# Performance work log

Hardware: AMD Instinct MI355X
Metric: run time of the kernel (lower is better)

The kernel has to match this reference:

```python
import jax, jax.numpy as jnp
import numpy as np

D_MODEL = 1024
D_INNER = 2048   # expand * d_model
D_STATE = 16
DT_RANK = 64     # ceil(d_model / 16)
D_CONV = 4
L = 2048
EPS = 1e-5


def setup_inputs() -> dict:
    key = jax.random.key(0)
    ks = jax.random.split(key, 8)
    sc = lambda k, shape: jax.random.normal(k, shape, jnp.float32) * 0.02
    A = jnp.tile(jnp.arange(1, D_STATE + 1, dtype=jnp.float32), (D_INNER, 1))
    return {
        "x": jax.random.normal(ks[0], (L, D_MODEL), jnp.float32),
        "W_in": sc(ks[1], (D_MODEL, 2 * D_INNER)),          # in_proj (no bias)
        "W_conv": sc(ks[2], (D_CONV, D_INNER)),             # depthwise conv kernel
        "b_conv": jnp.zeros((D_INNER,), jnp.float32),
        "W_x": sc(ks[3], (D_INNER, DT_RANK + 2 * D_STATE)), # x_proj (no bias)
        "W_dt": sc(ks[4], (DT_RANK, D_INNER)),
        "b_dt": jnp.zeros((D_INNER,), jnp.float32),
        "A_log": jnp.log(A),
        "D": jnp.ones((D_INNER,), jnp.float32),
        "W_out": sc(ks[5], (D_INNER, D_MODEL)),             # out_proj (no bias)
        "ln_scale": jnp.ones((D_MODEL,), jnp.float32),
        "ln_bias": jnp.zeros((D_MODEL,), jnp.float32),
        "drop_key": 0,  # unused: training=False -> DropPath is identity
    }


def reference(x, W_in, W_conv, b_conv, W_x, W_dt, b_dt, A_log, D, W_out,
              ln_scale, ln_bias, drop_key):
    l = x.shape[0]
    # LayerNorm (flax default: mean/var over features)
    mu = jnp.mean(x, axis=-1, keepdims=True)
    var = jnp.mean(jnp.square(x), axis=-1, keepdims=True) - jnp.square(mu)
    xn = (x - mu) * jax.lax.rsqrt(var + EPS) * ln_scale + ln_bias

    # MambaBlock
    xr = xn @ W_in                         # (l, 2*d_inner)
    u, res = xr[:, :D_INNER], xr[:, D_INNER:]

    # causal depthwise conv: pad left d_conv-1, take first l outputs
    up = jnp.pad(u, ((D_CONV - 1, 0), (0, 0)))
    uc = b_conv + sum(up[k:k + l] * W_conv[k] for k in range(D_CONV))
    u2 = jax.nn.silu(uc)                   # (l, d_inner)

    # SSM params (input-dependent)
    x_dbl = u2 @ W_x                       # (l, dt_rank + 2n)
    dt = x_dbl[:, :DT_RANK]
    B = x_dbl[:, DT_RANK:DT_RANK + D_STATE]
    C = x_dbl[:, DT_RANK + D_STATE:]
    delta = jax.nn.softplus(dt @ W_dt + b_dt)   # (l, d_inner)
    A = -jnp.exp(A_log)                         # (d_inner, n)

    dA = jnp.exp(jnp.einsum('ld,dn->ldn', delta, A))   # (l, d_inner, n)
    dBu = jnp.einsum('ld,ln->ldn', delta * u2, B)       # (l, d_inner, n)

    def step(h, inp):
        dA_t, dBu_t, C_t = inp
        h = dA_t * h + dBu_t               # (d_inner, n)
        return h, h @ C_t                  # y_t: (d_inner,)

    h0 = jnp.zeros((D_INNER, D_STATE), dtype=u2.dtype)
    _, ys = jax.lax.scan(step, h0, (dA, dBu, C))
    y = ys + u2 * D                        # (l, d_inner)

    y = y * jax.nn.silu(res)
    out = y @ W_out                        # (l, d_model)
    return out + x                         # residual (DropPath identity in eval)
```

## Files before the change

kernel.cpp:

```cpp
#include <hip/hip_runtime.h>
#include <math.h>

#define L_SEQ 2048
#define DM 1024
#define DI 2048
#define DS 16
#define DTR 64
#define EPS 1e-5f
#define NSEG 32
#define SEGLEN 64
#define NSTATE (DI * DS)

typedef float f32x4 __attribute__((ext_vector_type(4)));
typedef __bf16 bf16x8 __attribute__((ext_vector_type(8)));
typedef _Float16 h16x2 __attribute__((ext_vector_type(2)));

static __device__ __forceinline__ unsigned short f2bf(float f) {
  union { float f; unsigned u; } v; v.f = f;
  unsigned r = v.u + 0x7fffu + ((v.u >> 16) & 1u);
  return (unsigned short)(r >> 16);
}
static __device__ __forceinline__ float bf2f(unsigned short s) {
  union { unsigned u; float f; } v; v.u = ((unsigned)s) << 16;
  return v.f;
}

static __device__ __forceinline__ void gload16(const void* g, void* l) {
  __builtin_amdgcn_global_load_lds(
      (__attribute__((address_space(1))) void*)(unsigned long long)(g),
      (__attribute__((address_space(3))) void*)(unsigned)(unsigned long long)(l),
      16, 0, 0);
}

__global__ __launch_bounds__(256) void ln_kernel(const float* __restrict__ x,
                                                 const float* __restrict__ sc,
                                                 const float* __restrict__ bi,
                                                 unsigned short* __restrict__ xnb) {
  int row = blockIdx.x;
  int t = threadIdx.x;
  float4 xv = ((const float4*)(x + (size_t)row * DM))[t];
  float s  = xv.x + xv.y + xv.z + xv.w;
  float s2 = xv.x*xv.x + xv.y*xv.y + xv.z*xv.z + xv.w*xv.w;
  #pragma unroll
  for (int m = 32; m >= 1; m >>= 1) {
    s  += __shfl_xor(s, m);
    s2 += __shfl_xor(s2, m);
  }
  __shared__ float red[8];
  int wid = t >> 6, lane = t & 63;
  if (lane == 0) { red[wid] = s; red[4 + wid] = s2; }
  __syncthreads();
  s  = red[0] + red[1] + red[2] + red[3];
  s2 = red[4] + red[5] + red[6] + red[7];
  float mu = s * (1.f / DM);
  float var = s2 * (1.f / DM) - mu * mu;
  float rs = rsqrtf(var + EPS);
  float4 sc4 = ((const float4*)sc)[t];
  float4 bi4 = ((const float4*)bi)[t];
  ushort4 ob;
  ob.x = f2bf((xv.x - mu) * rs * sc4.x + bi4.x);
  ob.y = f2bf((xv.y - mu) * rs * sc4.y + bi4.y);
  ob.z = f2bf((xv.z - mu) * rs * sc4.z + bi4.z);
  ob.w = f2bf((xv.w - mu) * rs * sc4.w + bi4.w);
  *(ushort4*)&xnb[(size_t)row * DM + t * 4] = ob;
}

static __device__ __forceinline__ void trans_tile(
    const float* __restrict__ W, unsigned short* __restrict__ Wt,
    int K, int N, int n0, int k0)
{
  __shared__ unsigned short s[64][80];
  int tid = threadIdx.x;
  #pragma unroll
  for (int p = 0; p < 4; ++p) {
    int i = p * 16 + (tid >> 4);
    int j = (tid & 15) * 4;
    float4 w = *(const float4*)&W[(size_t)(k0 + i) * N + n0 + j];
    s[j + 0][i] = f2bf(w.x); s[j + 1][i] = f2bf(w.y);
    s[j + 2][i] = f2bf(w.z); s[j + 3][i] = f2bf(w.w);
  }
  __syncthreads();
  #pragma unroll
  for (int q = 0; q < 2; ++q) {
    int n = q * 32 + (tid >> 3);
    int i8 = (tid & 7) * 8;
    *(int4*)&Wt[(size_t)(n0 + n) * K + k0 + i8] = *(const int4*)&s[n][i8];
  }
}

__global__ __launch_bounds__(256) void prep_weights(
    const float* __restrict__ W_in, const float* __restrict__ W_out,
    const float* __restrict__ W_dt, const float* __restrict__ Wx,
    unsigned short* __restrict__ Wtin, unsigned short* __restrict__ Wtout,
    unsigned short* __restrict__ Wdt_t, unsigned short* __restrict__ Wxt)
{
  int b = blockIdx.x;
  if (b < 1024) {
    trans_tile(W_in, Wtin, DM, 2 * DI, (b & 63) * 64, (b >> 6) * 64);
  } else if (b < 1536) {
    int r = b - 1024;
    trans_tile(W_out, Wtout, DI, DM, (r & 15) * 64, (r >> 4) * 64);
  } else if (b < 1568) {
    int r = b - 1536;
    trans_tile(W_dt, Wdt_t, DTR, DI, r * 64, 0);
  } else {
    int r = b - 1568;
    int i = r * 256 + threadIdx.x;
    #pragma unroll
    for (int p = 0; p < 64; ++p) {
      int ii = i + p * 4096;
      int n = ii >> 11, k = ii & 2047;
      Wxt[ii] = (n < 96) ? f2bf(Wx[(size_t)k * 96 + n]) : (unsigned short)0;
    }
  }
}

template<int BM, int BN, int EPI, int OUTB, int SPLITK>
__global__ __launch_bounds__(256) void gemm2(
    const unsigned short* __restrict__ A, int lda,
    const unsigned short* __restrict__ Bt, int ldb,
    void* __restrict__ Cv, int ldc,
    int M, int N, int K,
    const float* __restrict__ bias)
{
  constexpr int WM = BM / 2, WN = BN / 2;
  constexpr int FM = WM / 16, FN = WN / 16;
  __shared__ __align__(16) unsigned short sm[(BM + BN) * 64];
  unsigned short* smA = sm;
  unsigned short* smB = sm + BM * 64;

  int nwg = gridDim.x * gridDim.y;
  int bid = blockIdx.y * gridDim.x + blockIdx.x;
  if ((nwg & 7) == 0) {
    int cpx = nwg >> 3;
    bid = (bid & 7) * cpx + (bid >> 3);
  }
  int bx = bid % gridDim.x;
  int by = bid / gridDim.x;
  int m0 = by * BM, n0 = bx * BN;

  int tid = threadIdx.x;
  int lane = tid & 63, wid = tid >> 6;
  int wm = wid >> 1, wn = wid & 1;

  int kb = blockIdx.z * (K / SPLITK);
  int nt = (K / SPLITK) / 64;

  int rs = lane >> 3;
  int cs = (lane & 7) * 8;

  f32x4 acc[FM][FN];
  #pragma unroll
  for (int m = 0; m < FM; ++m)
    #pragma unroll
    for (int n = 0; n < FN; ++n) acc[m][n] = (f32x4){0.f, 0.f, 0.f, 0.f};

  for (int kt = 0; kt < nt; ++kt) {
    __syncthreads();
    #pragma unroll
    for (int i = 0; i < BM / 32; ++i) {
      int chunk = wid * (BM / 32) + i;
      gload16(A + (size_t)(m0 + chunk * 8 + rs) * lda + kb + kt * 64 + cs,
              (char*)smA + chunk * 1024);
    }
    #pragma unroll
    for (int i = 0; i < BN / 32; ++i) {
      int chunk = wid * (BN / 32) + i;
      gload16(Bt + (size_t)(n0 + chunk * 8 + rs) * ldb + kb + kt * 64 + cs,
              (char*)smB + chunk * 1024);
    }
    __syncthreads();

    #pragma unroll
    for (int kk = 0; kk < 2; ++kk) {
      bf16x8 aF[FM], bF[FN];
      #pragma unroll
      for (int m = 0; m < FM; ++m) {
        int r = wm * WM + m * 16 + (lane & 15);
        aF[m] = *(const bf16x8*)((const char*)smA + r * 128 + kk * 64 + (lane >> 4) * 16);
      }
      #pragma unroll
      for (int n = 0; n < FN; ++n) {
        int r = wn * WN + n * 16 + (lane & 15);
        bF[n] = *(const bf16x8*)((const char*)smB + r * 128 + kk * 64 + (lane >> 4) * 16);
      }
      #pragma unroll
      for (int m = 0; m < FM; ++m)
        #pragma unroll
        for (int n = 0; n < FN; ++n)
          acc[m][n] = __builtin_amdgcn_mfma_f32_16x16x32_bf16(
              aF[m], bF[n], acc[m][n], 0, 0, 0);
    }
  }

  int cm = (lane >> 4) * 4, cn = lane & 15;
  if (OUTB) {
    unsigned short* Cb = (unsigned short*)Cv;
    __syncthreads();
    #pragma unroll
    for (int m = 0; m < FM; ++m)
      #pragma unroll
      for (int n = 0; n < FN; ++n) {
        int col = wn * WN + n * 16 + cn;
        #pragma unroll
        for (int r = 0; r < 4; ++r) {
          int row = wm * WM + m * 16 + cm + r;
          float v = acc[m][n][r];
          if (EPI == 1) {
            float w = v + bias[m0 + row];
            v = (w > 20.f) ? w : log1pf(__expf(w));
          }
          sm[row * BN + col] = f2bf(v);
        }
      }
    __syncthreads();
    constexpr int NI4 = BM * BN / 8;
    for (int k = tid; k < NI4; k += 256) {
      int row = k / (BN / 8);
      int c8 = (k % (BN / 8)) * 8;
      *(int4*)&Cb[(size_t)(m0 + row) * ldc + n0 + c8] = *(const int4*)&sm[row * BN + c8];
    }
  } else {
    float* Cf = (float*)Cv + (size_t)blockIdx.z * M * ldc;
    #pragma unroll
    for (int m = 0; m < FM; ++m)
      #pragma unroll
      for (int n = 0; n < FN; ++n) {
        int col = n0 + wn * WN + n * 16 + cn;
        #pragma unroll
        for (int r = 0; r < 4; ++r) {
          int row = m0 + wm * WM + m * 16 + cm + r;
          float v = acc[m][n][r];
          if (EPI == 1) {
            float w = v + bias[row];
            v = (w > 20.f) ? w : log1pf(__expf(w));
          }
          Cf[(size_t)row * ldc + col] = v;
        }
      }
  }
}

__global__ __launch_bounds__(256) void xdbl_reduce(
    const float* __restrict__ part, unsigned short* __restrict__ xdbl)
{
  int i = (blockIdx.x * 256 + threadIdx.x) * 4;
  const int SL = 2048 * 128;
  float4 s = *(const float4*)&part[i];
  #pragma unroll
  for (int z = 1; z < 16; ++z) {
    float4 p = *(const float4*)&part[(size_t)z * SL + i];
    s.x += p.x; s.y += p.y; s.z += p.z; s.w += p.w;
  }
  ushort4 ob;
  ob.x = f2bf(s.x); ob.y = f2bf(s.y); ob.z = f2bf(s.z); ob.w = f2bf(s.w);
  *(ushort4*)&xdbl[i] = ob;
}

__global__ __launch_bounds__(256) void out_reduce(
    const float* __restrict__ part, const float* __restrict__ x,
    float* __restrict__ out)
{
  int i = (blockIdx.x * 256 + threadIdx.x) * 4;
  const int SL = 2048 * 1024;
  float4 a = *(const float4*)&part[i];
  float4 b = *(const float4*)&part[SL + i];
  float4 r = *(const float4*)&x[i];
  float4 o;
  o.x = a.x + b.x + r.x; o.y = a.y + b.y + r.y;
  o.z = a.z + b.z + r.z; o.w = a.w + b.w + r.w;
  *(float4*)&out[i] = o;
}

__global__ __launch_bounds__(256) void conv_silu_fused(
    const unsigned short* __restrict__ xrT,
    const float* __restrict__ Wc, const float* __restrict__ bc,
    unsigned short* __restrict__ u2T, unsigned short* __restrict__ u2b)
{
  __shared__ unsigned short st[128][68];
  int d0 = blockIdx.x * 64, l0 = blockIdx.y * 128;
  int tid = threadIdx.x;
  int dloc = tid & 63;
  int lp = (tid >> 6) * 32;
  int d = d0 + dloc;
  const unsigned short* ur = xrT + (size_t)d * L_SEQ + l0 + lp;
  float w0 = Wc[0 * DI + d], w1 = Wc[1 * DI + d];
  float w2 = Wc[2 * DI + d], w3 = Wc[3 * DI + d];
  float b = bc[d];

  ushort4 vin[8];
  #pragma unroll
  for (int j = 0; j < 8; ++j) vin[j] = *(const ushort4*)&ur[j * 4];
  ushort4 vh; vh.x = vh.y = vh.z = vh.w = 0;
  if (l0 + lp > 0) vh = *(const ushort4*)&ur[-4];
  float prev3 = bf2f(vh.y), prev2 = bf2f(vh.z), prev1 = bf2f(vh.w);

  #pragma unroll
  for (int j = 0; j < 8; ++j) {
    float xs[4] = {bf2f(vin[j].x), bf2f(vin[j].y), bf2f(vin[j].z), bf2f(vin[j].w)};
    ushort4 ob;
    unsigned short* o = (unsigned short*)&ob;
    #pragma unroll
    for (int i = 0; i < 4; ++i) {
      float y = b + w0 * prev3 + w1 * prev2 + w2 * prev1 + w3 * xs[i];
      prev3 = prev2; prev2 = prev1; prev1 = xs[i];
      float sig = 1.f / (1.f + __expf(-y));
      o[i] = f2bf(y * sig);
    }
    *(ushort4*)&u2T[(size_t)d * L_SEQ + l0 + lp + j * 4] = ob;
    st[lp + j * 4 + 0][dloc] = o[0];
    st[lp + j * 4 + 1][dloc] = o[1];
    st[lp + j * 4 + 2][dloc] = o[2];
    st[lp + j * 4 + 3][dloc] = o[3];
  }
  __syncthreads();
  int lr = tid >> 1, hf = (tid & 1) * 32;
  unsigned short* ob = &u2b[(size_t)(l0 + lr) * DI + d0 + hf];
  *(int4*)&ob[0]  = *(const int4*)&st[lr][hf + 0];
  *(int4*)&ob[8]  = *(const int4*)&st[lr][hf + 8];
  *(int4*)&ob[16] = *(const int4*)&st[lr][hf + 16];
  *(int4*)&ob[24] = *(const int4*)&st[lr][hf + 24];
}


__global__ __launch_bounds__(128) void scan_pass1(
    const unsigned short* __restrict__ deltaT, const unsigned short* __restrict__ u2T,
    const unsigned short* __restrict__ xdbl,
    const float* __restrict__ A_log,
    float* __restrict__ hend, float* __restrict__ aprod)
{
  int t = threadIdx.x;
  int ch = t >> 4, n = t & 15;
  int li = (t & 15) * 4;
  int d0 = blockIdx.x * 8, d = d0 + ch;
  int base = blockIdx.y * SEGLEN;

  __shared__ __align__(16) float sdT[8][68], suT[8][68], sBT[16][68];

  float An = -__expf(A_log[d * DS + n]);

  ushort4 rdu = *(const ushort4*)&deltaT[(size_t)d * L_SEQ + base + li];
  ushort4 ru  = *(const ushort4*)&u2T[(size_t)d * L_SEQ + base + li];
  ushort4 rB[2];
  #pragma unroll
  for (int q = 0; q < 2; ++q) {
    int ll = base + (t >> 2) + q * 32;
    rB[q] = *(const ushort4*)&xdbl[(size_t)ll * 128 + 64 + (t & 3) * 4];
  }

  float d0v = bf2f(rdu.x), d1v = bf2f(rdu.y), d2v = bf2f(rdu.z), d3v = bf2f(rdu.w);
  sdT[ch][li + 0] = d0v; sdT[ch][li + 1] = d1v;
  sdT[ch][li + 2] = d2v; sdT[ch][li + 3] = d3v;
  suT[ch][li + 0] = d0v * bf2f(ru.x); suT[ch][li + 1] = d1v * bf2f(ru.y);
  suT[ch][li + 2] = d2v * bf2f(ru.z); suT[ch][li + 3] = d3v * bf2f(ru.w);
  #pragma unroll
  for (int q = 0; q < 2; ++q) {
    int ll = (t >> 2) + q * 32;
    int nb = (t & 3) * 4;
    sBT[nb + 0][ll] = bf2f(rB[q].x); sBT[nb + 1][ll] = bf2f(rB[q].y);
    sBT[nb + 2][ll] = bf2f(rB[q].z); sBT[nb + 3][ll] = bf2f(rB[q].w);
  }
  __syncthreads();

  float h = 0.f, sdl = 0.f;
  #pragma unroll
  for (int g = 0; g < 64; g += 4) {
    float4 dl4 = *(const float4*)&sdT[ch][g];
    float4 du4 = *(const float4*)&suT[ch][g];
    float4 Bn4 = *(const float4*)&sBT[n][g];
    float dl[4] = {dl4.x, dl4.y, dl4.z, dl4.w};
    float du[4] = {du4.x, du4.y, du4.z, du4.w};
    float Bn[4] = {Bn4.x, Bn4.y, Bn4.z, Bn4.w};
    #pragma unroll
    for (int i = 0; i < 4; ++i) {
      float dA = __expf(dl[i] * An);
      sdl += dl[i];
      h = dA * h + du[i] * Bn[i];
    }
  }
  size_t idx = (size_t)blockIdx.y * NSTATE + d0 * DS + t;
  hend[idx]  = h;
  aprod[idx] = __expf(An * sdl);
}

__global__ __launch_bounds__(256) void scan_pass2(
    const float* __restrict__ hend, const float* __restrict__ aprod,
    float* __restrict__ h_in)
{
  int i = blockIdx.x * 256 + threadIdx.x;
  float h = 0.f;
  h_in[i] = 0.f;
  for (int s = 0; s < NSEG - 1; ++s) {
    h = aprod[(size_t)s * NSTATE + i] * h + hend[(size_t)s * NSTATE + i];
    h_in[(size_t)(s + 1) * NSTATE + i] = h;
  }
}

__global__ __launch_bounds__(128) void scan_pass3(
    const unsigned short* __restrict__ deltaT, const unsigned short* __restrict__ u2T,
    const unsigned short* __restrict__ resT,
    const unsigned short* __restrict__ xdbl,
    const float* __restrict__ A_log, const float* __restrict__ Dp,
    const float* __restrict__ h_in,
    unsigned short* __restrict__ yb)
{
  int t = threadIdx.x;
  int ch = t >> 4, n = t & 15;
  int li = (t & 15) * 4;
  int d0 = blockIdx.x * 8, d = d0 + ch;
  int s = blockIdx.y;
  int base = s * SEGLEN;

  __shared__ __align__(16) float sdT[8][68], suT[8][68];
  __shared__ __align__(16) float sBT[16][68], sCT[16][68];
  __shared__ __align__(4) _Float16 svh[32][134];
  __shared__ __align__(16) unsigned short syt[32][8];

  float An = -__expf(A_log[d * DS + n]);
  float h = h_in[(size_t)s * NSTATE + d0 * DS + t];

  ushort4 rdu = *(const ushort4*)&deltaT[(size_t)d * L_SEQ + base + li];
  ushort4 ru  = *(const ushort4*)&u2T[(size_t)d * L_SEQ + base + li];
  ushort4 rB[2], rC[2];
  #pragma unroll
  for (int q = 0; q < 2; ++q) {
    int ll = base + (t >> 2) + q * 32;
    int n4 = (t & 3) * 4;
    rB[q] = *(const ushort4*)&xdbl[(size_t)ll * 128 + 64 + n4];
    rC[q] = *(const ushort4*)&xdbl[(size_t)ll * 128 + 80 + n4];
  }

  float d0v = bf2f(rdu.x), d1v = bf2f(rdu.y), d2v = bf2f(rdu.z), d3v = bf2f(rdu.w);
  sdT[ch][li + 0] = d0v; sdT[ch][li + 1] = d1v;
  sdT[ch][li + 2] = d2v; sdT[ch][li + 3] = d3v;
  suT[ch][li + 0] = d0v * bf2f(ru.x); suT[ch][li + 1] = d1v * bf2f(ru.y);
  suT[ch][li + 2] = d2v * bf2f(ru.z); suT[ch][li + 3] = d3v * bf2f(ru.w);
  #pragma unroll
  for (int q = 0; q < 2; ++q) {
    int ll = (t >> 2) + q * 32;
    int nb = (t & 3) * 4;
    sBT[nb + 0][ll] = bf2f(rB[q].x); sBT[nb + 1][ll] = bf2f(rB[q].y);
    sBT[nb + 2][ll] = bf2f(rB[q].z); sBT[nb + 3][ll] = bf2f(rB[q].w);
    sCT[nb + 0][ll] = bf2f(rC[q].x); sCT[nb + 1][ll] = bf2f(rC[q].y);
    sCT[nb + 2][ll] = bf2f(rC[q].z); sCT[nb + 3][ll] = bf2f(rC[q].w);
  }
  __syncthreads();

  #pragma unroll
  for (int half = 0; half < 2; ++half) {
    int g0 = half * 32;
    #pragma unroll
    for (int g = g0; g < g0 + 32; g += 4) {
      float4 dl4 = *(const float4*)&sdT[ch][g];
      float4 du4 = *(const float4*)&suT[ch][g];
      float4 Bn4 = *(const float4*)&sBT[n][g];
      float4 Cn4 = *(const float4*)&sCT[n][g];
      float dl[4] = {dl4.x, dl4.y, dl4.z, dl4.w};
      float du[4] = {du4.x, du4.y, du4.z, du4.w};
      float Bn[4] = {Bn4.x, Bn4.y, Bn4.z, Bn4.w};
      float Cn[4] = {Cn4.x, Cn4.y, Cn4.z, Cn4.w};
      #pragma unroll
      for (int i = 0; i < 4; ++i) {
        float dA = __expf(dl[i] * An);
        h = dA * h + du[i] * Bn[i];
        svh[g - g0 + i][t] = (_Float16)(h * Cn[i]);
      }
    }
    __syncthreads();

    #pragma unroll
    for (int r = 0; r < 2; ++r) {
      int idx = r * 128 + t;
      int ll = idx & 31, c2 = idx >> 5;
      const _Float16* row = &svh[ll][c2 * 16];
      float sum = 0.f;
      #pragma unroll
      for (int k = 0; k < 8; ++k) {
        h16x2 pv = *(const h16x2*)&row[k * 2];
        sum += (float)pv.x + (float)pv.y;
      }
      int dd = d0 + c2;
      int lg = base + g0 + ll;
      float uv = bf2f(u2T[(size_t)dd * L_SEQ + lg]);
      float rv = bf2f(resT[(size_t)dd * L_SEQ + lg]);
      float sig = 1.f / (1.f + __expf(-rv));
      syt[ll][c2] = f2bf((sum + uv * Dp[dd]) * rv * sig);
    }
    __syncthreads();
    if (t < 32) {
      int lg = base + g0 + t;
      *(int4*)&yb[(size_t)lg * DI + d0] = *(const int4*)&syt[t][0];
    }
  }
}

extern "C" void kernel_launch(void* const* d_in, const int* in_sizes, int n_in,
                              void* d_out, int out_size, void* d_ws, size_t ws_size,
                              hipStream_t stream)
{
  const float* x      = (const float*)d_in[0];
  const float* W_in   = (const float*)d_in[1];
  const float* W_conv = (const float*)d_in[2];
  const float* b_conv = (const float*)d_in[3];
  const float* W_x    = (const float*)d_in[4];
  const float* W_dt   = (const float*)d_in[5];
  const float* b_dt   = (const float*)d_in[6];
  const float* A_log  = (const float*)d_in[7];
  const float* Dp     = (const float*)d_in[8];
  const float* W_out  = (const float*)d_in[9];
  const float* ln_s   = (const float*)d_in[10];
  const float* ln_b   = (const float*)d_in[11];

  char* ws = (char*)d_ws;
  const size_t MB = 1u << 20;
  unsigned short* xnb    = (unsigned short*)(ws);
  unsigned short* xrT    = (unsigned short*)(ws + 4 * MB);
  unsigned short* u2T    = (unsigned short*)(ws + 20 * MB);
  unsigned short* u2b    = (unsigned short*)(ws + 28 * MB);
  float*          hend   = (float*)(ws + 28 * MB);
  float*          aprod  = (float*)(ws + 32 * MB);
  unsigned short* xdbl   = (unsigned short*)(ws + 36 * MB);
  unsigned short* Wxt    = (unsigned short*)(ws + 36 * MB + 512 * 1024);
  unsigned short* Wdt_t  = (unsigned short*)(ws + 37 * MB);
  unsigned short* deltaTb= (unsigned short*)(ws + 38 * MB);
  unsigned short* Wtin   = (unsigned short*)(ws + 38 * MB);
  float*          part   = (float*)(ws + 46 * MB);
  float*          h_in   = (float*)(ws + 62 * MB);
  unsigned short* Wtout  = (unsigned short*)(ws + 66 * MB);
  unsigned short* yb     = (unsigned short*)(ws + 4 * MB);
  const unsigned short* resT = xrT + (size_t)DI * L_SEQ;

  prep_weights<<<1584, 256, 0, stream>>>(W_in, W_out, W_dt, W_x,
                                          Wtin, Wtout, Wdt_t, Wxt);

  ln_kernel<<<L_SEQ, 256, 0, stream>>>(x, ln_s, ln_b, xnb);

  gemm2<128, 128, 0, 1, 1><<<dim3(L_SEQ / 128, (2 * DI) / 128), 256, 0, stream>>>(
      Wtin, DM, xnb, DM, xrT, L_SEQ, 2 * DI, L_SEQ, DM, nullptr);

  conv_silu_fused<<<dim3(DI / 64, L_SEQ / 128), 256, 0, stream>>>(
      xrT, W_conv, b_conv, u2T, u2b);

  gemm2<64, 128, 0, 0, 16><<<dim3(1, L_SEQ / 64, 16), 256, 0, stream>>>(
      u2b, DI, Wxt, DI, part, 128, L_SEQ, 128, DI, nullptr);

  xdbl_reduce<<<(L_SEQ * 128) / 1024, 256, 0, stream>>>(part, xdbl);

  gemm2<64, 128, 1, 1, 1><<<dim3(L_SEQ / 128, DI / 64), 256, 0, stream>>>(
      Wdt_t, DTR, xdbl, 128, deltaTb, L_SEQ, DI, L_SEQ, DTR, b_dt);

  scan_pass1<<<dim3(DI / 8, NSEG - 1), 128, 0, stream>>>(
      deltaTb, u2T, xdbl, A_log, hend, aprod);

  scan_pass2<<<NSTATE / 256, 256, 0, stream>>>(hend, aprod, h_in);

  scan_pass3<<<dim3(DI / 8, NSEG), 128, 0, stream>>>(
      deltaTb, u2T, resT, xdbl, A_log, Dp, h_in, yb);

  gemm2<64, 128, 0, 0, 2><<<dim3(DM / 128, L_SEQ / 64, 2), 256, 0, stream>>>(
      yb, DI, Wtout, DI, part, DM, L_SEQ, DM, DI, nullptr);

  out_reduce<<<(L_SEQ * DM) / 1024, 256, 0, stream>>>(part, x, (float*)d_out);
}
```

Baseline: 178.4 us.

## Fuse layernorm into weight prep and residual add into out-proj GEMM epilogue

Merges the layernorm kernel into the weight-prep kernel as extra blocks, saving one launch. Replaces the split-K out-projection plus separate reduce kernel with a single non-split 64x64-tile GEMM whose epilogue adds the residual x and writes the output directly, removing the partial-sum round trip through memory. Also halves the split-K factor of the x_proj GEMM, so the reduction has fewer partials to read. The trade-off is less K-parallelism in both GEMMs, with smaller tiles and longer per-block K loops.

```diff
diff --git a/kernel.cpp b/kernel.cpp
--- a/kernel.cpp
+++ b/kernel.cpp
@@ -32,39 +32,6 @@
       16, 0, 0);
 }
 
-__global__ __launch_bounds__(256) void ln_kernel(const float* __restrict__ x,
-                                                 const float* __restrict__ sc,
-                                                 const float* __restrict__ bi,
-                                                 unsigned short* __restrict__ xnb) {
-  int row = blockIdx.x;
-  int t = threadIdx.x;
-  float4 xv = ((const float4*)(x + (size_t)row * DM))[t];
-  float s  = xv.x + xv.y + xv.z + xv.w;
-  float s2 = xv.x*xv.x + xv.y*xv.y + xv.z*xv.z + xv.w*xv.w;
-  #pragma unroll
-  for (int m = 32; m >= 1; m >>= 1) {
-    s  += __shfl_xor(s, m);
-    s2 += __shfl_xor(s2, m);
-  }
-  __shared__ float red[8];
-  int wid = t >> 6, lane = t & 63;
-  if (lane == 0) { red[wid] = s; red[4 + wid] = s2; }
-  __syncthreads();
-  s  = red[0] + red[1] + red[2] + red[3];
-  s2 = red[4] + red[5] + red[6] + red[7];
-  float mu = s * (1.f / DM);
-  float var = s2 * (1.f / DM) - mu * mu;
-  float rs = rsqrtf(var + EPS);
-  float4 sc4 = ((const float4*)sc)[t];
-  float4 bi4 = ((const float4*)bi)[t];
-  ushort4 ob;
-  ob.x = f2bf((xv.x - mu) * rs * sc4.x + bi4.x);
-  ob.y = f2bf((xv.y - mu) * rs * sc4.y + bi4.y);
-  ob.z = f2bf((xv.z - mu) * rs * sc4.z + bi4.z);
-  ob.w = f2bf((xv.w - mu) * rs * sc4.w + bi4.w);
-  *(ushort4*)&xnb[(size_t)row * DM + t * 4] = ob;
-}
-
 static __device__ __forceinline__ void trans_tile(
     const float* __restrict__ W, unsigned short* __restrict__ Wt,
     int K, int N, int n0, int k0)
@@ -88,24 +55,55 @@
   }
 }
 
-__global__ __launch_bounds__(256) void prep_weights(
+__global__ __launch_bounds__(256) void prep_all(
+    const float* __restrict__ x, const float* __restrict__ ln_s,
+    const float* __restrict__ ln_b, unsigned short* __restrict__ xnb,
     const float* __restrict__ W_in, const float* __restrict__ W_out,
     const float* __restrict__ W_dt, const float* __restrict__ Wx,
     unsigned short* __restrict__ Wtin, unsigned short* __restrict__ Wtout,
     unsigned short* __restrict__ Wdt_t, unsigned short* __restrict__ Wxt)
 {
   int b = blockIdx.x;
-  if (b < 1024) {
-    trans_tile(W_in, Wtin, DM, 2 * DI, (b & 63) * 64, (b >> 6) * 64);
-  } else if (b < 1536) {
-    int r = b - 1024;
+  int t = threadIdx.x;
+  if (b < 2048) {
+    __shared__ float red[8];
+    int row = b;
+    float4 xv = ((const float4*)(x + (size_t)row * DM))[t];
+    float s  = xv.x + xv.y + xv.z + xv.w;
+    float s2 = xv.x*xv.x + xv.y*xv.y + xv.z*xv.z + xv.w*xv.w;
+    #pragma unroll
+    for (int m = 32; m >= 1; m >>= 1) {
+      s  += __shfl_xor(s, m);
+      s2 += __shfl_xor(s2, m);
+    }
+    int wid = t >> 6, lane = t & 63;
+    if (lane == 0) { red[wid] = s; red[4 + wid] = s2; }
+    __syncthreads();
+    s  = red[0] + red[1] + red[2] + red[3];
+    s2 = red[4] + red[5] + red[6] + red[7];
+    float mu = s * (1.f / DM);
+    float var = s2 * (1.f / DM) - mu * mu;
+    float rs = rsqrtf(var + EPS);
+    float4 sc4 = ((const float4*)ln_s)[t];
+    float4 bi4 = ((const float4*)ln_b)[t];
+    ushort4 ob;
+    ob.x = f2bf((xv.x - mu) * rs * sc4.x + bi4.x);
+    ob.y = f2bf((xv.y - mu) * rs * sc4.y + bi4.y);
+    ob.z = f2bf((xv.z - mu) * rs * sc4.z + bi4.z);
+    ob.w = f2bf((xv.w - mu) * rs * sc4.w + bi4.w);
+    *(ushort4*)&xnb[(size_t)row * DM + t * 4] = ob;
+  } else if (b < 3072) {
+    int r = b - 2048;
+    trans_tile(W_in, Wtin, DM, 2 * DI, (r & 63) * 64, (r >> 6) * 64);
+  } else if (b < 3584) {
+    int r = b - 3072;
     trans_tile(W_out, Wtout, DI, DM, (r & 15) * 64, (r >> 4) * 64);
-  } else if (b < 1568) {
-    int r = b - 1536;
+  } else if (b < 3616) {
+    int r = b - 3584;
     trans_tile(W_dt, Wdt_t, DTR, DI, r * 64, 0);
   } else {
-    int r = b - 1568;
-    int i = r * 256 + threadIdx.x;
+    int r = b - 3616;
+    int i = r * 256 + t;
     #pragma unroll
     for (int p = 0; p < 64; ++p) {
       int ii = i + p * 4096;
@@ -121,7 +119,8 @@
     const unsigned short* __restrict__ Bt, int ldb,
     void* __restrict__ Cv, int ldc,
     int M, int N, int K,
-    const float* __restrict__ bias)
+    const float* __restrict__ bias,
+    const float* __restrict__ R, int ldr)
 {
   constexpr int WM = BM / 2, WN = BN / 2;
   constexpr int FM = WM / 16, FN = WN / 16;
@@ -235,6 +234,7 @@
             float w = v + bias[row];
             v = (w > 20.f) ? w : log1pf(__expf(w));
           }
+          if (EPI == 2) v += R[(size_t)row * ldr + col];
           Cf[(size_t)row * ldc + col] = v;
         }
       }
@@ -248,28 +248,13 @@
   const int SL = 2048 * 128;
   float4 s = *(const float4*)&part[i];
   #pragma unroll
-  for (int z = 1; z < 16; ++z) {
+  for (int z = 1; z < 8; ++z) {
     float4 p = *(const float4*)&part[(size_t)z * SL + i];
     s.x += p.x; s.y += p.y; s.z += p.z; s.w += p.w;
   }
   ushort4 ob;
   ob.x = f2bf(s.x); ob.y = f2bf(s.y); ob.z = f2bf(s.z); ob.w = f2bf(s.w);
   *(ushort4*)&xdbl[i] = ob;
-}
-
-__global__ __launch_bounds__(256) void out_reduce(
-    const float* __restrict__ part, const float* __restrict__ x,
-    float* __restrict__ out)
-{
-  int i = (blockIdx.x * 256 + threadIdx.x) * 4;
-  const int SL = 2048 * 1024;
-  float4 a = *(const float4*)&part[i];
-  float4 b = *(const float4*)&part[SL + i];
-  float4 r = *(const float4*)&x[i];
-  float4 o;
-  o.x = a.x + b.x + r.x; o.y = a.y + b.y + r.y;
-  o.z = a.z + b.z + r.z; o.w = a.w + b.w + r.w;
-  *(float4*)&out[i] = o;
 }
 
 __global__ __launch_bounds__(256) void conv_silu_fused(
@@ -530,24 +515,23 @@
   unsigned short* yb     = (unsigned short*)(ws + 4 * MB);
   const unsigned short* resT = xrT + (size_t)DI * L_SEQ;
 
-  prep_weights<<<1584, 256, 0, stream>>>(W_in, W_out, W_dt, W_x,
-                                          Wtin, Wtout, Wdt_t, Wxt);
-
-  ln_kernel<<<L_SEQ, 256, 0, stream>>>(x, ln_s, ln_b, xnb);
+  prep_all<<<3632, 256, 0, stream>>>(x, ln_s, ln_b, xnb,
+                                     W_in, W_out, W_dt, W_x,
+                                     Wtin, Wtout, Wdt_t, Wxt);
 
   gemm2<128, 128, 0, 1, 1><<<dim3(L_SEQ / 128, (2 * DI) / 128), 256, 0, stream>>>(
-      Wtin, DM, xnb, DM, xrT, L_SEQ, 2 * DI, L_SEQ, DM, nullptr);
+      Wtin, DM, xnb, DM, xrT, L_SEQ, 2 * DI, L_SEQ, DM, nullptr, nullptr, 0);
 
   conv_silu_fused<<<dim3(DI / 64, L_SEQ / 128), 256, 0, stream>>>(
       xrT, W_conv, b_conv, u2T, u2b);
 
-  gemm2<64, 128, 0, 0, 16><<<dim3(1, L_SEQ / 64, 16), 256, 0, stream>>>(
-      u2b, DI, Wxt, DI, part, 128, L_SEQ, 128, DI, nullptr);
+  gemm2<64, 128, 0, 0, 8><<<dim3(1, L_SEQ / 64, 8), 256, 0, stream>>>(
+      u2b, DI, Wxt, DI, part, 128, L_SEQ, 128, DI, nullptr, nullptr, 0);
 
   xdbl_reduce<<<(L_SEQ * 128) / 1024, 256, 0, stream>>>(part, xdbl);
 
   gemm2<64, 128, 1, 1, 1><<<dim3(L_SEQ / 128, DI / 64), 256, 0, stream>>>(
-      Wdt_t, DTR, xdbl, 128, deltaTb, L_SEQ, DI, L_SEQ, DTR, b_dt);
+      Wdt_t, DTR, xdbl, 128, deltaTb, L_SEQ, DI, L_SEQ, DTR, b_dt, nullptr, 0);
 
   scan_pass1<<<dim3(DI / 8, NSEG - 1), 128, 0, stream>>>(
       deltaTb, u2T, xdbl, A_log, hend, aprod);
@@ -557,8 +541,6 @@
   scan_pass3<<<dim3(DI / 8, NSEG), 128, 0, stream>>>(
       deltaTb, u2T, resT, xdbl, A_log, Dp, h_in, yb);
 
-  gemm2<64, 128, 0, 0, 2><<<dim3(DM / 128, L_SEQ / 64, 2), 256, 0, stream>>>(
-      yb, DI, Wtout, DI, part, DM, L_SEQ, DM, DI, nullptr);
-
-  out_reduce<<<(L_SEQ * DM) / 1024, 256, 0, stream>>>(part, x, (float*)d_out);
-}
+  gemm2<64, 64, 2, 0, 1><<<dim3(DM / 64, L_SEQ / 64), 256, 0, stream>>>(
+      yb, DI, Wtout, DI, (float*)d_out, DM, L_SEQ, DM, DI, nullptr, x, DM);
+}
```

New measurement: 180.4 us. No clear change (+1.1%).
